# Optimization experiments

Measured on AMD Instinct MI355X. Metric: run time of the kernel, lower is better.

Reference implementation:

```python
import jax, jax.numpy as jnp
import numpy as np

B, NIN, NREG, D, H, L = 8, 1024, 16, 1024, 16, 12
DFF = 4 * D
S = NIN + NREG
HD = D // H
EPS = 1e-6


def setup_inputs() -> dict:
    key = jax.random.key(0)
    ks = jax.random.split(key, 8)
    p = lambda k, shape: jax.random.normal(k, shape, jnp.float32) * 0.02
    return dict(
        x=jax.random.normal(ks[0], (B, S, D), jnp.float32),
        n_input=NIN,
        ln1_g=jnp.ones((L, D), jnp.float32), ln1_b=jnp.zeros((L, D), jnp.float32),
        wqkv=p(ks[1], (L, D, 3 * D)), bqkv=jnp.zeros((L, 3 * D), jnp.float32),
        wo=p(ks[2], (L, D, D)), bo=jnp.zeros((L, D), jnp.float32),
        ln2_g=jnp.ones((L, D), jnp.float32), ln2_b=jnp.zeros((L, D), jnp.float32),
        w1=p(ks[3], (L, D, DFF)), b1=jnp.zeros((L, DFF), jnp.float32),
        w2=p(ks[4], (L, DFF, D)), b2=jnp.zeros((L, D), jnp.float32),
        lnf_g=jnp.ones((D,), jnp.float32), lnf_b=jnp.zeros((D,), jnp.float32),
    )


def _ln(x, g, b):
    mu = x.mean(-1, keepdims=True)
    var = ((x - mu) ** 2).mean(-1, keepdims=True)
    return (x - mu) * jax.lax.rsqrt(var + EPS) * g + b


def _build_mask(n_input, total):
    # inputs attend everywhere; registers attend to all inputs and causally among registers
    i = jnp.arange(total)[:, None]
    j = jnp.arange(total)[None, :]
    blocked = (i >= n_input) & (j >= n_input) & (j > i)
    return jnp.where(blocked, -jnp.inf, 0.0).astype(jnp.float32)  # (S, S) additive


def _attn(h, wqkv_l, bqkv_l, wo_l, bo_l, mask):
    b, s, _ = h.shape
    qkv = h @ wqkv_l + bqkv_l                                   # (B,S,3D)
    q, k, v = jnp.split(qkv, 3, axis=-1)
    q = q.reshape(b, s, H, HD).transpose(0, 2, 1, 3)            # (B,H,S,HD)
    k = k.reshape(b, s, H, HD).transpose(0, 2, 1, 3)
    v = v.reshape(b, s, H, HD).transpose(0, 2, 1, 3)
    scores = jnp.einsum('bhqd,bhkd->bhqk', q, k) / np.sqrt(HD) + mask
    a = jax.nn.softmax(scores, axis=-1)
    o = jnp.einsum('bhqk,bhkd->bhqd', a, v)
    o = o.transpose(0, 2, 1, 3).reshape(b, s, D)
    return o @ wo_l + bo_l


def reference(x, n_input, ln1_g, ln1_b, wqkv, bqkv, wo, bo,
              ln2_g, ln2_b, w1, b1, w2, b2, lnf_g, lnf_b):
    mask = _build_mask(n_input, x.shape[1])

    def blk(h, p):
        l1g, l1b, wq, bq, wo_, bo_, l2g, l2b, w1_, b1_, w2_, b2_ = p
        h = h + _attn(_ln(h, l1g, l1b), wq, bq, wo_, bo_, mask)
        u = _ln(h, l2g, l2b) @ w1_ + b1_
        h = h + jax.nn.gelu(u) @ w2_ + b2_
        return h, None

    h, _ = jax.lax.scan(blk, x, (ln1_g, ln1_b, wqkv, bqkv, wo, bo,
                                 ln2_g, ln2_b, w1, b1, w2, b2))
    return _ln(h, lnf_g, lnf_b)
```

## Files before the change

### kernel.cpp

```cpp
#include <hip/hip_runtime.h>
#include <hip/hip_bf16.h>
#include <stdint.h>

#define DD   1024
#define TD   3072
#define DFFN 4096
#define NL   12
#define SS   1040
#define SP   1056
#define BB   8
#define MM   (BB*SS)
#define HH   16
#define NTAIL 32

typedef float  f32x4  __attribute__((ext_vector_type(4)));
typedef __bf16 bf16x8 __attribute__((ext_vector_type(8)));
typedef unsigned short u16;

union Bf8 { bf16x8 v; u16 s[8]; };

__device__ __forceinline__ u16 f2b(float f) {
  union { float f; unsigned u; } x; x.f = f;
  unsigned r = (x.u + 0x7FFFu + ((x.u >> 16) & 1u)) >> 16;
  return (u16)r;
}

__device__ __forceinline__ f32x4 mfma_bf16(bf16x8 a, bf16x8 b, f32x4 c) {
  return __builtin_amdgcn_mfma_f32_16x16x32_bf16(a, b, c, 0, 0, 0);
}

__device__ __forceinline__ void gload_lds16(const u16* g, u16* l) {
  __builtin_amdgcn_global_load_lds((const __attribute__((address_space(1))) void*)g,
                                   (__attribute__((address_space(3))) void*)l, 16, 0, 0);
}

__device__ __forceinline__ float dppmax16(float t) {
  union { float f; int i; } u, v;
  u.f = t;
  v.i = __builtin_amdgcn_update_dpp(0, u.i, 0xB1, 0xF, 0xF, true);
  u.f = fmaxf(u.f, v.f);
  v.i = __builtin_amdgcn_update_dpp(0, u.i, 0x4E, 0xF, 0xF, true);
  u.f = fmaxf(u.f, v.f);
  v.i = __builtin_amdgcn_update_dpp(0, u.i, 0x124, 0xF, 0xF, true);
  u.f = fmaxf(u.f, v.f);
  v.i = __builtin_amdgcn_update_dpp(0, u.i, 0x128, 0xF, 0xF, true);
  u.f = fmaxf(u.f, v.f);
  return u.f;
}

__global__ __launch_bounds__(256)
void transpose_cast(const float* __restrict__ in, u16* __restrict__ out, int K, int N) {
  __shared__ float tile[32][33];
  const int n0 = blockIdx.x * 32, k0 = blockIdx.y * 32;
  const size_t lb = (size_t)blockIdx.z * K * N;
  const int tx = threadIdx.x, ty = threadIdx.y;
  for (int j = 0; j < 4; ++j)
    tile[ty + 8*j][tx] = in[lb + (size_t)(k0 + ty + 8*j) * N + n0 + tx];
  __syncthreads();
  for (int j = 0; j < 4; ++j)
    out[lb + (size_t)(n0 + ty + 8*j) * K + k0 + tx] = f2b(tile[tx][ty + 8*j]);
}

__global__ __launch_bounds__(256)
void ln_kernel(const float* __restrict__ in, const float* __restrict__ gam,
               const float* __restrict__ bet, u16* __restrict__ outb) {
  const int row = blockIdx.x, t = threadIdx.x;
  const float4 v = ((const float4*)(in + (size_t)row * DD))[t];
  float s  = v.x + v.y + v.z + v.w;
  float s2 = v.x*v.x + v.y*v.y + v.z*v.z + v.w*v.w;
  for (int off = 1; off < 64; off <<= 1) { s += __shfl_xor(s, off); s2 += __shfl_xor(s2, off); }
  __shared__ float red[8];
  if ((t & 63) == 0) { red[t >> 6] = s; red[4 + (t >> 6)] = s2; }
  __syncthreads();
  s  = red[0] + red[1] + red[2] + red[3];
  s2 = red[4] + red[5] + red[6] + red[7];
  const float mu = s * (1.0f/1024.0f);
  const float var = s2 * (1.0f/1024.0f) - mu*mu;
  const float rs = rsqrtf(var + 1e-6f);
  const float4 gv = ((const float4*)gam)[t];
  const float4 bv = ((const float4*)bet)[t];
  ushort4 o;
  o.x = f2b((v.x - mu)*rs*gv.x + bv.x);
  o.y = f2b((v.y - mu)*rs*gv.y + bv.y);
  o.z = f2b((v.z - mu)*rs*gv.z + bv.z);
  o.w = f2b((v.w - mu)*rs*gv.w + bv.w);
  ((ushort4*)(outb + (size_t)row * DD))[t] = o;
}

template<int OUTF>
__global__ __launch_bounds__(256)
void ln_comb(const float* __restrict__ P0, const float* __restrict__ P1,
             float* __restrict__ hout, const float* __restrict__ gam,
             const float* __restrict__ bet, u16* __restrict__ outb,
             float* __restrict__ outf) {
  const int row = blockIdx.x, t = threadIdx.x;
  const float4 a = ((const float4*)(P0 + (size_t)row * DD))[t];
  const float4 b = ((const float4*)(P1 + (size_t)row * DD))[t];
  float4 v; v.x = a.x + b.x; v.y = a.y + b.y; v.z = a.z + b.z; v.w = a.w + b.w;
  ((float4*)(hout + (size_t)row * DD))[t] = v;
  float s  = v.x + v.y + v.z + v.w;
  float s2 = v.x*v.x + v.y*v.y + v.z*v.z + v.w*v.w;
  for (int off = 1; off < 64; off <<= 1) { s += __shfl_xor(s, off); s2 += __shfl_xor(s2, off); }
  __shared__ float red[8];
  if ((t & 63) == 0) { red[t >> 6] = s; red[4 + (t >> 6)] = s2; }
  __syncthreads();
  s  = red[0] + red[1] + red[2] + red[3];
  s2 = red[4] + red[5] + red[6] + red[7];
  const float mu = s * (1.0f/1024.0f);
  const float var = s2 * (1.0f/1024.0f) - mu*mu;
  const float rs = rsqrtf(var + 1e-6f);
  const float4 gv = ((const float4*)gam)[t];
  const float4 bv = ((const float4*)bet)[t];
  const float y0 = (v.x - mu)*rs*gv.x + bv.x;
  const float y1 = (v.y - mu)*rs*gv.y + bv.y;
  const float y2 = (v.z - mu)*rs*gv.z + bv.z;
  const float y3 = (v.w - mu)*rs*gv.w + bv.w;
  if (OUTF) {
    float4 o; o.x=y0; o.y=y1; o.z=y2; o.w=y3;
    ((float4*)(outf + (size_t)row * DD))[t] = o;
  } else {
    ushort4 o; o.x=f2b(y0); o.y=f2b(y1); o.z=f2b(y2); o.w=f2b(y3);
    ((ushort4*)(outb + (size_t)row * DD))[t] = o;
  }
}

template<int EPI>
__global__ __launch_bounds__(256, 4)
void gemm_bt(const u16* __restrict__ A, const u16* __restrict__ Bt,
             const float* __restrict__ bias, const float* __restrict__ resid,
             float* outF, u16* outB,
             u16* __restrict__ qb, u16* __restrict__ kb, u16* __restrict__ vtb,
             int N, int K) {
  __shared__ u16 As[128*64];
  __shared__ u16 Bs[128*64];
  const int tid = threadIdx.x;

  const int nwg = gridDim.x * gridDim.y;
  int wgid = blockIdx.y * gridDim.x + blockIdx.x;
  wgid = (wgid & 7) * (nwg >> 3) + (wgid >> 3);
  const int nb = wgid % gridDim.y;
  const int mb = wgid / gridDim.y;
  const int m0 = mb * 128, n0 = nb * 128;

  const int lane = tid & 63, w = tid >> 6;
  const int wr = (w >> 1) * 64, wc = (w & 1) * 64;
  const int c = lane & 15, g = lane >> 4;

  f32x4 acc[4][4];
  for (int i = 0; i < 4; ++i) for (int j = 0; j < 4; ++j) acc[i][j] = f32x4{0.f,0.f,0.f,0.f};

  const int srow = tid >> 3, scg = tid & 7;
  const size_t aoff = (size_t)(m0 + srow) * K + scg * 8;
  const size_t boff = (size_t)(n0 + srow) * K + scg * 8;

  for (int kt = 0; kt < K; kt += 64) {
    for (int it = 0; it < 4; ++it) {
      gload_lds16(A  + aoff + (size_t)it * 32 * K + kt, As + (it*256 + tid) * 8);
      gload_lds16(Bt + boff + (size_t)it * 32 * K + kt, Bs + (it*256 + tid) * 8);
    }
    __syncthreads();
    for (int kk = 0; kk < 2; ++kk) {
      bf16x8 af[4], bfr[4];
      for (int i = 0; i < 4; ++i) af[i]  = *(const bf16x8*)(As + (wr + i*16 + c)*64 + kk*32 + g*8);
      for (int j = 0; j < 4; ++j) bfr[j] = *(const bf16x8*)(Bs + (wc + j*16 + c)*64 + kk*32 + g*8);
      for (int i = 0; i < 4; ++i)
        for (int j = 0; j < 4; ++j)
          acc[i][j] = mfma_bf16(af[i], bfr[j], acc[i][j]);
    }
    __syncthreads();
  }

  for (int j = 0; j < 4; ++j) {
    const int col = n0 + wc + j*16 + c;
    const float bcol = bias[col];
    for (int i = 0; i < 4; ++i) {
      const int row0 = m0 + wr + i*16 + 4*g;
      if (EPI == 3) {
        const int part = col >> 10;
        const int hh2  = (col >> 6) & 15;
        const int hd   = col & 63;
        const int bb   = (int)((unsigned)row0 / SS);
        const int s0   = row0 - bb * SS;
        const size_t bh = (size_t)(bb * HH + hh2);
        if (part == 2) {
          ushort4 pk;
          pk.x = f2b(acc[i][j][0] + bcol);
          pk.y = f2b(acc[i][j][1] + bcol);
          pk.z = f2b(acc[i][j][2] + bcol);
          pk.w = f2b(acc[i][j][3] + bcol);
          *(ushort4*)(vtb + (bh*64 + hd)*SP + s0) = pk;
        } else if (part == 0) {
          for (int r = 0; r < 4; ++r)
            qb[(bh*SP + s0 + r)*64 + hd] = f2b((acc[i][j][r] + bcol) * 0.125f);
        } else {
          for (int r = 0; r < 4; ++r)
            kb[(bh*SP + s0 + r)*64 + hd] = f2b(acc[i][j][r] + bcol);
        }
      } else {
        for (int r = 0; r < 4; ++r) {
          const size_t idx = (size_t)(row0 + r) * N + col;
          const float v = acc[i][j][r] + bcol;
          if (EPI == 1) {
            const float z = 1.5957691216f * (v + 0.044715f * v * v * v);
            const float e = __expf(z);
            outB[idx] = f2b(v * e * __builtin_amdgcn_rcpf(e + 1.0f));
          } else {
            outF[idx] = v + resid[idx];
          }
        }
      }
    }
  }
}

__global__ __launch_bounds__(256, 4)
void gemm_ffn2(const u16* __restrict__ A, const u16* __restrict__ Bt,
               const float* __restrict__ bias, const float* __restrict__ resid,
               float* __restrict__ P0, float* __restrict__ P1, int N, int K) {
  __shared__ u16 As[128*64];
  __shared__ u16 Bs[128*64];
  const int tid = threadIdx.x;
  const int kh = blockIdx.z;

  const int nwg = gridDim.x * gridDim.y;
  int wgid = blockIdx.y * gridDim.x + blockIdx.x;
  wgid = (wgid & 7) * (nwg >> 3) + (wgid >> 3);
  const int nb = wgid % gridDim.y;
  const int mb = wgid / gridDim.y;
  const int m0 = mb * 128, n0 = nb * 128;

  const int lane = tid & 63, w = tid >> 6;
  const int wr = (w >> 1) * 64, wc = (w & 1) * 64;
  const int c = lane & 15, g = lane >> 4;

  f32x4 acc[4][4];
  for (int i = 0; i < 4; ++i) for (int j = 0; j < 4; ++j) acc[i][j] = f32x4{0.f,0.f,0.f,0.f};

  const int KH = K >> 1;
  const int srow = tid >> 3, scg = tid & 7;
  const size_t aoff = (size_t)(m0 + srow) * K + scg * 8 + (size_t)kh * KH;
  const size_t boff = (size_t)(n0 + srow) * K + scg * 8 + (size_t)kh * KH;

  for (int kt = 0; kt < KH; kt += 64) {
    for (int it = 0; it < 4; ++it) {
      gload_lds16(A  + aoff + (size_t)it * 32 * K + kt, As + (it*256 + tid) * 8);
      gload_lds16(Bt + boff + (size_t)it * 32 * K + kt, Bs + (it*256 + tid) * 8);
    }
    __syncthreads();
    for (int kk = 0; kk < 2; ++kk) {
      bf16x8 af[4], bfr[4];
      for (int i = 0; i < 4; ++i) af[i]  = *(const bf16x8*)(As + (wr + i*16 + c)*64 + kk*32 + g*8);
      for (int j = 0; j < 4; ++j) bfr[j] = *(const bf16x8*)(Bs + (wc + j*16 + c)*64 + kk*32 + g*8);
      for (int i = 0; i < 4; ++i)
        for (int j = 0; j < 4; ++j)
          acc[i][j] = mfma_bf16(af[i], bfr[j], acc[i][j]);
    }
    __syncthreads();
  }

  float* outP = kh ? P1 : P0;
  for (int j = 0; j < 4; ++j) {
    const int col = n0 + wc + j*16 + c;
    const float bcol = kh ? 0.f : bias[col];
    for (int i = 0; i < 4; ++i) {
      const int row0 = m0 + wr + i*16 + 4*g;
      for (int r = 0; r < 4; ++r) {
        const size_t idx = (size_t)(row0 + r) * N + col;
        float v = acc[i][j][r] + bcol;
        if (!kh) v += resid[idx];
        outP[idx] = v;
      }
    }
  }
}

__global__ __launch_bounds__(256, 4)
void gemm64(const u16* __restrict__ A, const u16* __restrict__ Bt,
            const float* __restrict__ bias, const float* __restrict__ resid,
            float* __restrict__ outF, int N, int K) {
  __shared__ u16 As[64*64];
  __shared__ u16 Bs[128*64];
  const int tid = threadIdx.x;

  const int nwg = gridDim.x * gridDim.y;
  int wgid = blockIdx.y * gridDim.x + blockIdx.x;
  wgid = (wgid & 7) * (nwg >> 3) + (wgid >> 3);
  const int nb = wgid % gridDim.y;
  const int mb = wgid / gridDim.y;
  const int m0 = mb * 64, n0 = nb * 128;

  const int lane = tid & 63, w = tid >> 6;
  const int wr = (w >> 1) * 32, wc = (w & 1) * 64;
  const int c = lane & 15, g = lane >> 4;

  f32x4 acc[2][4];
  for (int i = 0; i < 2; ++i) for (int j = 0; j < 4; ++j) acc[i][j] = f32x4{0.f,0.f,0.f,0.f};

  const int srow = tid >> 3, scg = tid & 7;
  const size_t aoff = (size_t)(m0 + srow) * K + scg * 8;
  const size_t boff = (size_t)(n0 + srow) * K + scg * 8;

  for (int kt = 0; kt < K; kt += 64) {
    for (int it = 0; it < 2; ++it)
      gload_lds16(A  + aoff + (size_t)it * 32 * K + kt, As + (it*256 + tid) * 8);
    for (int it = 0; it < 4; ++it)
      gload_lds16(Bt + boff + (size_t)it * 32 * K + kt, Bs + (it*256 + tid) * 8);
    __syncthreads();
    for (int kk = 0; kk < 2; ++kk) {
      bf16x8 af[2], bfr[4];
      for (int i = 0; i < 2; ++i) af[i]  = *(const bf16x8*)(As + (wr + i*16 + c)*64 + kk*32 + g*8);
      for (int j = 0; j < 4; ++j) bfr[j] = *(const bf16x8*)(Bs + (wc + j*16 + c)*64 + kk*32 + g*8);
      for (int i = 0; i < 2; ++i)
        for (int j = 0; j < 4; ++j)
          acc[i][j] = mfma_bf16(af[i], bfr[j], acc[i][j]);
    }
    __syncthreads();
  }

  for (int j = 0; j < 4; ++j) {
    const int col = n0 + wc + j*16 + c;
    const float bcol = bias[col];
    for (int i = 0; i < 2; ++i) {
      const int row0 = m0 + wr + i*16 + 4*g;
      for (int r = 0; r < 4; ++r) {
        const size_t idx = (size_t)(row0 + r) * N + col;
        outF[idx] = acc[i][j][r] + bcol + resid[idx];
      }
    }
  }
}

__global__ __launch_bounds__(256, 4)
void attn_staged(const u16* __restrict__ Qb, const u16* __restrict__ Kb,
                 const u16* __restrict__ VTb, u16* __restrict__ out,
                 const int* __restrict__ npt) {
  __shared__ u16 KV[2][4096];
  __shared__ u16 PT[4][640];
  const int tid = threadIdx.x;
  const int w = tid >> 6, lane = tid & 63;
  const int c = lane & 15, g = lane >> 4;
  const int nin = npt[0];
  u16* pw = PT[w];

  if (blockIdx.x < NTAIL) {
    const int bh = blockIdx.x * 4 + w;
    const int b = bh >> 4, hh = bh & 15;
    const int q0 = 64 * 16;

    bf16x8 aq0, aq1;
    {
      const u16* qp = Qb + ((size_t)bh * SP + q0 + c) * 64 + g * 8;
      aq0 = *(const bf16x8*)qp;
      aq1 = *(const bf16x8*)(qp + 32);
    }

    float m[4], ls[4];
    f32x4 o[4];
    int qrow[4];
    for (int r = 0; r < 4; ++r) { m[r] = -1e30f; ls[r] = 0.f; qrow[r] = q0 + 4*g + r; }
    for (int nd = 0; nd < 4; ++nd) o[nd] = f32x4{0.f,0.f,0.f,0.f};

    for (int kt = 0; kt < 33; ++kt) {
      const int k0 = kt * 32;

      f32x4 s[2];
      {
        const u16* kp0 = Kb + ((size_t)bh * SP + k0 + c) * 64 + g * 8;
        f32x4 z0 = f32x4{0.f,0.f,0.f,0.f};
        z0 = mfma_bf16(aq0, *(const bf16x8*)kp0, z0);
        z0 = mfma_bf16(aq1, *(const bf16x8*)(kp0 + 32), z0);
        s[0] = z0;
        const u16* kp1 = kp0 + 16 * 64;
        f32x4 z1 = f32x4{0.f,0.f,0.f,0.f};
        z1 = mfma_bf16(aq0, *(const bf16x8*)kp1, z1);
        z1 = mfma_bf16(aq1, *(const bf16x8*)(kp1 + 32), z1);
        s[1] = z1;
      }

      for (int jt = 0; jt < 2; ++jt) {
        const int j = k0 + jt*16 + c;
        for (int r = 0; r < 4; ++r) {
          const int q = qrow[r];
          const bool blocked = (j >= SS) || ((q >= nin) && (j >= nin) && (j > q));
          if (blocked) s[jt][r] = -1e30f;
        }
      }

      for (int r = 0; r < 4; ++r) {
        float t = fmaxf(s[0][r], s[1][r]);
        for (int off = 1; off < 16; off <<= 1) t = fmaxf(t, __shfl_xor(t, off));
        const float mn = fmaxf(m[r], t);
        const float al = __expf(m[r] - mn);
        m[r] = mn;
        const float p0 = __expf(s[0][r] - mn);
        const float p1 = __expf(s[1][r] - mn);
        s[0][r] = p0; s[1][r] = p1;
        float ps = p0 + p1;
        for (int off = 1; off < 16; off <<= 1) ps += __shfl_xor(ps, off);
        ls[r] = ls[r] * al + ps;
        for (int nd = 0; nd < 4; ++nd) o[nd][r] *= al;
      }

      for (int jt = 0; jt < 2; ++jt)
        for (int r = 0; r < 4; ++r)
          pw[(4*g + r)*40 + jt*16 + c] = f2b(s[jt][r]);
      __builtin_amdgcn_sched_barrier(0);
      bf16x8 ap = *(const bf16x8*)(pw + c*40 + 8*g);
      __builtin_amdgcn_sched_barrier(0);

      for (int nd = 0; nd < 4; ++nd) {
        const u16* vp = VTb + ((size_t)bh * 64 + nd*16 + c) * SP + k0 + 8*g;
        o[nd] = mfma_bf16(ap, *(const bf16x8*)vp, o[nd]);
      }
    }

    for (int nd = 0; nd < 4; ++nd)
      for (int r = 0; r < 4; ++r) {
        const float v = o[nd][r] / ls[r];
        out[((size_t)b * SS + qrow[r]) * DD + hh*64 + nd*16 + c] = f2b(v);
      }
    return;
  }

  const int sb = blockIdx.x - NTAIL;
  const int bh = sb & 127;
  const int qg = sb >> 7;
  const int b = bh >> 4, hh = bh & 15;

  const u16 *ssrc0, *ssrc1; int kstr; u16 *sdst0, *sdst1;
  if (tid < 128) {
    const int i0 = tid, i1 = tid + 128;
    const int r0 = i0 >> 3, cg0 = (i0 & 7) ^ (r0 & 7);
    const int r1 = i1 >> 3, cg1 = (i1 & 7) ^ (r1 & 7);
    ssrc0 = Kb + ((size_t)bh * SP + r0) * 64 + cg0 * 8;
    ssrc1 = Kb + ((size_t)bh * SP + r1) * 64 + cg1 * 8;
    kstr = 32 * 64;
    sdst0 = &KV[0][i0 * 8];
    sdst1 = &KV[0][i1 * 8];
  } else {
    const int t2 = tid - 128;
    const int i0 = t2, i1 = t2 + 128;
    const int r0 = i0 >> 2, cg0 = (i0 & 3) ^ (r0 & 3);
    const int r1 = i1 >> 2, cg1 = (i1 & 3) ^ (r1 & 3);
    ssrc0 = VTb + ((size_t)bh * 64 + r0) * SP + cg0 * 8;
    ssrc1 = VTb + ((size_t)bh * 64 + r1) * SP + cg1 * 8;
    kstr = 32;
    sdst0 = &KV[0][2048 + i0 * 8];
    sdst1 = &KV[0][2048 + i1 * 8];
  }
#define STAGE(bufbit, kt) do { \
    gload_lds16(ssrc0 + (size_t)(kt) * kstr, sdst0 + (bufbit) * 4096); \
    gload_lds16(ssrc1 + (size_t)(kt) * kstr, sdst1 + (bufbit) * 4096); } while (0)

  bf16x8 aq[2][2];
  int q0[2];
#pragma unroll
  for (int qq = 0; qq < 2; ++qq) {
    q0[qq] = (qg * 8 + w * 2 + qq) * 16;
    const u16* qp = Qb + ((size_t)bh * SP + q0[qq] + c) * 64 + g * 8;
    aq[qq][0] = *(const bf16x8*)qp;
    aq[qq][1] = *(const bf16x8*)(qp + 32);
  }

  Bf8 onesf;
  for (int i = 0; i < 8; ++i) onesf.s[i] = (c == 0) ? (u16)0x3F80 : (u16)0;

  float m[2][4];
  f32x4 o[2][5];
#pragma unroll
  for (int qq = 0; qq < 2; ++qq) {
    for (int r = 0; r < 4; ++r) m[qq][r] = -1e30f;
    for (int nd = 0; nd < 5; ++nd) o[qq][nd] = f32x4{0.f,0.f,0.f,0.f};
  }
  const bool tregs0 = (q0[0] + 15) >= nin;
  const bool tregs1 = (q0[1] + 15) >= nin;
  const int c7 = c & 7, c3 = c & 3;

  STAGE(0, 0);

  for (int kt = 0; kt < 33; ++kt) {
    const int buf = kt & 1;
    __syncthreads();
    if (kt < 32) STAGE(buf ^ 1, kt + 1);
    const u16* Kt = &KV[buf][0];
    const u16* Vt = &KV[buf][2048];
    const int k0 = kt * 32;

    bf16x8 k00 = *(const bf16x8*)(Kt + c*64        + ((g    ) ^ c7) * 8);
    bf16x8 k01 = *(const bf16x8*)(Kt + c*64        + ((g + 4) ^ c7) * 8);
    bf16x8 k10 = *(const bf16x8*)(Kt + (c+16)*64   + ((g    ) ^ c7) * 8);
    bf16x8 k11 = *(const bf16x8*)(Kt + (c+16)*64   + ((g + 4) ^ c7) * 8);

#pragma unroll
    for (int qq = 0; qq < 2; ++qq) {
      f32x4 s[2];
      {
        f32x4 z0 = f32x4{0.f,0.f,0.f,0.f};
        z0 = mfma_bf16(aq[qq][0], k00, z0);
        z0 = mfma_bf16(aq[qq][1], k01, z0);
        s[0] = z0;
        f32x4 z1 = f32x4{0.f,0.f,0.f,0.f};
        z1 = mfma_bf16(aq[qq][0], k10, z1);
        z1 = mfma_bf16(aq[qq][1], k11, z1);
        s[1] = z1;
      }

      const bool tregs = qq ? tregs1 : tregs0;
      if (tregs || (k0 + 31 >= SS)) {
        const int qr0 = q0[qq] + 4*g;
        for (int jt = 0; jt < 2; ++jt) {
          const int j = k0 + jt*16 + c;
          for (int r = 0; r < 4; ++r) {
            const int q = qr0 + r;
            const bool blocked = (j >= SS) || ((q >= nin) && (j >= nin) && (j > q));
            if (blocked) s[jt][r] = -1e30f;
          }
        }
      }

      for (int r = 0; r < 4; ++r) {
        const float t = dppmax16(fmaxf(s[0][r], s[1][r]));
        const float mn = fmaxf(m[qq][r], t);
        const float al = __expf(m[qq][r] - mn);
        m[qq][r] = mn;
        for (int nd = 0; nd < 5; ++nd) o[qq][nd][r] *= al;
        s[0][r] = __expf(s[0][r] - mn);
        s[1][r] = __expf(s[1][r] - mn);
      }

      for (int jt = 0; jt < 2; ++jt)
        for (int r = 0; r < 4; ++r)
          pw[(4*g + r)*40 + jt*16 + c] = f2b(s[jt][r]);
      __builtin_amdgcn_sched_barrier(0);
      bf16x8 ap = *(const bf16x8*)(pw + c*40 + 8*g);
      __builtin_amdgcn_sched_barrier(0);

      for (int nd = 0; nd < 4; ++nd) {
        bf16x8 bv = *(const bf16x8*)(Vt + (nd*16 + c)*32 + ((g ^ c3) * 8));
        o[qq][nd] = mfma_bf16(ap, bv, o[qq][nd]);
      }
      o[qq][4] = mfma_bf16(ap, onesf.v, o[qq][4]);
    }
  }
#undef STAGE

#pragma unroll
  for (int qq = 0; qq < 2; ++qq) {
    float rls[4];
    for (int r = 0; r < 4; ++r)
      rls[r] = 1.0f / __shfl(o[qq][4][r], lane & 48);
    const int qr0 = q0[qq] + 4*g;
    for (int nd = 0; nd < 4; ++nd)
      for (int r = 0; r < 4; ++r)
        out[((size_t)b * SS + qr0 + r) * DD + hh*64 + nd*16 + c] = f2b(o[qq][nd][r] * rls[r]);
  }
}

extern "C" void kernel_launch(void* const* d_in, const int* in_sizes, int n_in,
                              void* d_out, int out_size, void* d_ws, size_t ws_size,
                              hipStream_t stream) {
  const float* x    = (const float*)d_in[0];
  const int*   npt  = (const int*)  d_in[1];
  const float* ln1g = (const float*)d_in[2];
  const float* ln1b = (const float*)d_in[3];
  const float* wqkv = (const float*)d_in[4];
  const float* bqkv = (const float*)d_in[5];
  const float* wo   = (const float*)d_in[6];
  const float* bo   = (const float*)d_in[7];
  const float* ln2g = (const float*)d_in[8];
  const float* ln2b = (const float*)d_in[9];
  const float* w1   = (const float*)d_in[10];
  const float* b1   = (const float*)d_in[11];
  const float* w2   = (const float*)d_in[12];
  const float* b2   = (const float*)d_in[13];
  const float* lnfg = (const float*)d_in[14];
  const float* lnfb = (const float*)d_in[15];

  char* ws = (char*)d_ws;
  size_t off = 0;
  u16*   wqkvT = (u16*)(ws + off);   off += (size_t)NL*TD*DD*2;
  u16*   woT   = (u16*)(ws + off);   off += (size_t)NL*DD*DD*2;
  u16*   w1T   = (u16*)(ws + off);   off += (size_t)NL*DFFN*DD*2;
  u16*   w2T   = (u16*)(ws + off);   off += (size_t)NL*DD*DFFN*2;
  float* h     = (float*)(ws + off); off += (size_t)MM*DD*4;
  u16*   lnb   = (u16*)(ws + off);   off += (size_t)MM*DD*2;
  u16*   Qb    = (u16*)(ws + off);   off += (size_t)BB*HH*SP*64*2;
  u16*   Kb    = (u16*)(ws + off);   off += (size_t)BB*HH*SP*64*2;
  u16*   VTb   = (u16*)(ws + off);   off += (size_t)BB*HH*64*SP*2;
  u16*   attnO = (u16*)(ws + off);   off += (size_t)MM*DD*2;
  u16*   ffh   = (u16*)(ws + off);   off += (size_t)MM*DFFN*2;
  float* P0    = (float*)(ws + off); off += (size_t)MM*DD*4;
  float* P1    = (float*)(ws + off); off += (size_t)MM*DD*4;

  const dim3 tb(32, 8);
  transpose_cast<<<dim3(TD/32,   DD/32,   NL), tb, 0, stream>>>(wqkv, wqkvT, DD,   TD);
  transpose_cast<<<dim3(DD/32,   DD/32,   NL), tb, 0, stream>>>(wo,   woT,   DD,   DD);
  transpose_cast<<<dim3(DFFN/32, DD/32,   NL), tb, 0, stream>>>(w1,   w1T,   DD,   DFFN);
  transpose_cast<<<dim3(DD/32,   DFFN/32, NL), tb, 0, stream>>>(w2,   w2T,   DFFN, DD);
  hipMemcpyAsync(h, x, (size_t)MM*DD*4, hipMemcpyDeviceToDevice, stream);
  hipMemsetAsync(Qb, 0, (size_t)3*BB*HH*SP*64*2, stream);

  for (int l = 0; l < NL; ++l) {
    if (l == 0)
      ln_kernel<<<MM, 256, 0, stream>>>(h, ln1g, ln1b, lnb);
    else
      ln_comb<0><<<MM, 256, 0, stream>>>(P0, P1, h, ln1g + (size_t)l*DD, ln1b + (size_t)l*DD,
                                         lnb, nullptr);
    gemm_bt<3><<<dim3(MM/128, TD/128), 256, 0, stream>>>(
        lnb, wqkvT + (size_t)l*TD*DD, bqkv + (size_t)l*TD, nullptr, nullptr, nullptr,
        Qb, Kb, VTb, TD, DD);
    attn_staged<<<dim3(1024 + NTAIL), 256, 0, stream>>>(Qb, Kb, VTb, attnO, npt);
    gemm64<<<dim3(MM/64, DD/128), 256, 0, stream>>>(
        attnO, woT + (size_t)l*DD*DD, bo + (size_t)l*DD, h, h, DD, DD);
    ln_kernel<<<MM, 256, 0, stream>>>(h, ln2g + (size_t)l*DD, ln2b + (size_t)l*DD, lnb);
    gemm_bt<1><<<dim3(MM/128, DFFN/128), 256, 0, stream>>>(
        lnb, w1T + (size_t)l*DFFN*DD, b1 + (size_t)l*DFFN, nullptr, nullptr, ffh,
        nullptr, nullptr, nullptr, DFFN, DD);
    gemm_ffn2<<<dim3(MM/128, DD/128, 2), 256, 0, stream>>>(
        ffh, w2T + (size_t)l*DD*DFFN, b2 + (size_t)l*DD, h, P0, P1, DD, DFFN);
  }
  ln_comb<1><<<MM, 256, 0, stream>>>(P0, P1, h, lnfg, lnfb, nullptr, (float*)d_out);
}
```

Before: 5.712 ms.

## Use split-K for output projection and skip softmax rescale unless max grows

The attention output projection now uses the 128x128 split-K GEMM, writing two partial sums. The second LayerNorm becomes ln_comb, which combines the partials and residual, and the gemm64 kernel and unused epilogue paths are removed. In attention, the running-max update and accumulator rescale now happen only when some row's block max exceeds the current max by more than 8 (lazy rescaling). Otherwise exponentials use the stale max. This trades fewer rescale multiplies and exps for partial-buffer traffic and possible fp range growth bounded by e^8.

Result: slower. 5.903 ms (+3.4%).

```diff
diff --git a/kernel.cpp b/kernel.cpp
--- a/kernel.cpp
+++ b/kernel.cpp
@@ -127,8 +127,8 @@
 template<int EPI>
 __global__ __launch_bounds__(256, 4)
 void gemm_bt(const u16* __restrict__ A, const u16* __restrict__ Bt,
-             const float* __restrict__ bias, const float* __restrict__ resid,
-             float* outF, u16* outB,
+             const float* __restrict__ bias,
+             u16* outB,
              u16* __restrict__ qb, u16* __restrict__ kb, u16* __restrict__ vtb,
              int N, int K) {
   __shared__ u16 As[128*64];
@@ -200,13 +200,9 @@
         for (int r = 0; r < 4; ++r) {
           const size_t idx = (size_t)(row0 + r) * N + col;
           const float v = acc[i][j][r] + bcol;
-          if (EPI == 1) {
-            const float z = 1.5957691216f * (v + 0.044715f * v * v * v);
-            const float e = __expf(z);
-            outB[idx] = f2b(v * e * __builtin_amdgcn_rcpf(e + 1.0f));
-          } else {
-            outF[idx] = v + resid[idx];
-          }
+          const float z = 1.5957691216f * (v + 0.044715f * v * v * v);
+          const float e = __expf(z);
+          outB[idx] = f2b(v * e * __builtin_amdgcn_rcpf(e + 1.0f));
         }
       }
     }
@@ -214,9 +210,9 @@
 }
 
 __global__ __launch_bounds__(256, 4)
-void gemm_ffn2(const u16* __restrict__ A, const u16* __restrict__ Bt,
-               const float* __restrict__ bias, const float* __restrict__ resid,
-               float* __restrict__ P0, float* __restrict__ P1, int N, int K) {
+void gemm_splitk(const u16* __restrict__ A, const u16* __restrict__ Bt,
+                 const float* __restrict__ bias, const float* __restrict__ resid,
+                 float* __restrict__ P0, float* __restrict__ P1, int N, int K) {
   __shared__ u16 As[128*64];
   __shared__ u16 Bs[128*64];
   const int tid = threadIdx.x;
@@ -269,62 +265,6 @@
         float v = acc[i][j][r] + bcol;
         if (!kh) v += resid[idx];
         outP[idx] = v;
-      }
-    }
-  }
-}
-
-__global__ __launch_bounds__(256, 4)
-void gemm64(const u16* __restrict__ A, const u16* __restrict__ Bt,
-            const float* __restrict__ bias, const float* __restrict__ resid,
-            float* __restrict__ outF, int N, int K) {
-  __shared__ u16 As[64*64];
-  __shared__ u16 Bs[128*64];
-  const int tid = threadIdx.x;
-
-  const int nwg = gridDim.x * gridDim.y;
-  int wgid = blockIdx.y * gridDim.x + blockIdx.x;
-  wgid = (wgid & 7) * (nwg >> 3) + (wgid >> 3);
-  const int nb = wgid % gridDim.y;
-  const int mb = wgid / gridDim.y;
-  const int m0 = mb * 64, n0 = nb * 128;
-
-  const int lane = tid & 63, w = tid >> 6;
-  const int wr = (w >> 1) * 32, wc = (w & 1) * 64;
-  const int c = lane & 15, g = lane >> 4;
-
-  f32x4 acc[2][4];
-  for (int i = 0; i < 2; ++i) for (int j = 0; j < 4; ++j) acc[i][j] = f32x4{0.f,0.f,0.f,0.f};
-
-  const int srow = tid >> 3, scg = tid & 7;
-  const size_t aoff = (size_t)(m0 + srow) * K + scg * 8;
-  const size_t boff = (size_t)(n0 + srow) * K + scg * 8;
-
-  for (int kt = 0; kt < K; kt += 64) {
-    for (int it = 0; it < 2; ++it)
-      gload_lds16(A  + aoff + (size_t)it * 32 * K + kt, As + (it*256 + tid) * 8);
-    for (int it = 0; it < 4; ++it)
-      gload_lds16(Bt + boff + (size_t)it * 32 * K + kt, Bs + (it*256 + tid) * 8);
-    __syncthreads();
-    for (int kk = 0; kk < 2; ++kk) {
-      bf16x8 af[2], bfr[4];
-      for (int i = 0; i < 2; ++i) af[i]  = *(const bf16x8*)(As + (wr + i*16 + c)*64 + kk*32 + g*8);
-      for (int j = 0; j < 4; ++j) bfr[j] = *(const bf16x8*)(Bs + (wc + j*16 + c)*64 + kk*32 + g*8);
-      for (int i = 0; i < 2; ++i)
-        for (int j = 0; j < 4; ++j)
-          acc[i][j] = mfma_bf16(af[i], bfr[j], acc[i][j]);
-    }
-    __syncthreads();
-  }
-
-  for (int j = 0; j < 4; ++j) {
-    const int col = n0 + wc + j*16 + c;
-    const float bcol = bias[col];
-    for (int i = 0; i < 2; ++i) {
-      const int row0 = m0 + wr + i*16 + 4*g;
-      for (int r = 0; r < 4; ++r) {
-        const size_t idx = (size_t)(row0 + r) * N + col;
-        outF[idx] = acc[i][j][r] + bcol + resid[idx];
       }
     }
   }
@@ -518,14 +458,22 @@
         }
       }
 
+      float t4[4];
+      for (int r = 0; r < 4; ++r)
+        t4[r] = dppmax16(fmaxf(s[0][r], s[1][r]));
+      const bool need = (t4[0] > m[qq][0] + 8.f) || (t4[1] > m[qq][1] + 8.f) ||
+                        (t4[2] > m[qq][2] + 8.f) || (t4[3] > m[qq][3] + 8.f);
+      if (__any(need)) {
+        for (int r = 0; r < 4; ++r) {
+          const float mn = fmaxf(m[qq][r], t4[r]);
+          const float al = __expf(m[qq][r] - mn);
+          m[qq][r] = mn;
+          for (int nd = 0; nd < 5; ++nd) o[qq][nd][r] *= al;
+        }
+      }
       for (int r = 0; r < 4; ++r) {
-        const float t = dppmax16(fmaxf(s[0][r], s[1][r]));
-        const float mn = fmaxf(m[qq][r], t);
-        const float al = __expf(m[qq][r] - mn);
-        m[qq][r] = mn;
-        for (int nd = 0; nd < 5; ++nd) o[qq][nd][r] *= al;
-        s[0][r] = __expf(s[0][r] - mn);
-        s[1][r] = __expf(s[1][r] - mn);
+        s[0][r] = __expf(s[0][r] - m[qq][r]);
+        s[1][r] = __expf(s[1][r] - m[qq][r]);
       }
 
       for (int jt = 0; jt < 2; ++jt)
@@ -607,16 +555,17 @@
       ln_comb<0><<<MM, 256, 0, stream>>>(P0, P1, h, ln1g + (size_t)l*DD, ln1b + (size_t)l*DD,
                                          lnb, nullptr);
     gemm_bt<3><<<dim3(MM/128, TD/128), 256, 0, stream>>>(
-        lnb, wqkvT + (size_t)l*TD*DD, bqkv + (size_t)l*TD, nullptr, nullptr, nullptr,
+        lnb, wqkvT + (size_t)l*TD*DD, bqkv + (size_t)l*TD, nullptr,
         Qb, Kb, VTb, TD, DD);
     attn_staged<<<dim3(1024 + NTAIL), 256, 0, stream>>>(Qb, Kb, VTb, attnO, npt);
-    gemm64<<<dim3(MM/64, DD/128), 256, 0, stream>>>(
-        attnO, woT + (size_t)l*DD*DD, bo + (size_t)l*DD, h, h, DD, DD);
-    ln_kernel<<<MM, 256, 0, stream>>>(h, ln2g + (size_t)l*DD, ln2b + (size_t)l*DD, lnb);
+    gemm_splitk<<<dim3(MM/128, DD/128, 2), 256, 0, stream>>>(
+        attnO, woT + (size_t)l*DD*DD, bo + (size_t)l*DD, h, P0, P1, DD, DD);
+    ln_comb<0><<<MM, 256, 0, stream>>>(P0, P1, h, ln2g + (size_t)l*DD, ln2b + (size_t)l*DD,
+                                       lnb, nullptr);
     gemm_bt<1><<<dim3(MM/128, DFFN/128), 256, 0, stream>>>(
-        lnb, w1T + (size_t)l*DFFN*DD, b1 + (size_t)l*DFFN, nullptr, nullptr, ffh,
+        lnb, w1T + (size_t)l*DFFN*DD, b1 + (size_t)l*DFFN, ffh,
         nullptr, nullptr, nullptr, DFFN, DD);
-    gemm_ffn2<<<dim3(MM/128, DD/128, 2), 256, 0, stream>>>(
+    gemm_splitk<<<dim3(MM/128, DD/128, 2), 256, 0, stream>>>(
         ffh, w2T + (size_t)l*DD*DFFN, b2 + (size_t)l*DD, h, P0, P1, DD, DFFN);
   }
   ln_comb<1><<<MM, 256, 0, stream>>>(P0, P1, h, lnfg, lnfb, nullptr, (float*)d_out);
```
